# Kernel tuning notes

Measured on AMD Instinct MI355X. Metric: run time of the kernel, lower is better.

Reference implementation:

```python
import jax, jax.numpy as jnp
import numpy as np

U, NB, I, D = 20000, 10000, 40000, 64
L = 2          # num_layers
H = 64         # fusion hidden
M = 40         # max bundle size
BATCH, K = 8192, 2
DEG_UI, DEG_UB = 30, 20


def _sym_block(r, c, nA, nB):
    """Build symmetric bipartite block [[0, A],[A^T, 0]] with laplace normalization."""
    rows = np.concatenate([r, c + nA])
    cols = np.concatenate([c + nA, r])
    n = nA + nB
    deg = np.bincount(rows, minlength=n).astype(np.float64)
    inv = 1.0 / (np.sqrt(deg) + 1e-8)
    vals = (inv[rows] * inv[cols]).astype(np.float32)
    return rows.astype(np.int32), cols.astype(np.int32), vals


def setup_inputs() -> dict:
    rng = np.random.default_rng(0)
    ui_r = np.repeat(np.arange(U), DEG_UI)
    ui_c = rng.integers(0, I, U * DEG_UI)
    il_rows, il_cols, il_vals = _sym_block(ui_r, ui_c, U, I)
    ub_r = np.repeat(np.arange(U), DEG_UB)
    ub_c = rng.integers(0, NB, U * DEG_UB)
    bl_rows, bl_cols, bl_vals = _sym_block(ub_r, ub_c, U, NB)
    lengths = rng.integers(10, M + 1, NB)
    bundle_item_ids = rng.integers(0, I, (NB, M)).astype(np.int32)
    bundle_item_mask = (np.arange(M)[None, :] < lengths[:, None])

    key = jax.random.key(0)
    ks = jax.random.split(key, 8)

    def xavier(k, shape):
        std = np.sqrt(2.0 / (shape[0] + shape[1])).astype(np.float32)
        return jax.random.normal(k, shape, dtype=jnp.float32) * std

    return {
        'users_feature': xavier(ks[0], (U, D)),
        'items_feature': xavier(ks[1], (I, D)),
        'bundles_feature': xavier(ks[2], (NB, D)),
        'fw1': xavier(ks[3], (2 * D, H)),
        'fb1': jnp.zeros((H,), jnp.float32),
        'fw2': xavier(ks[4], (H, 1)),
        'fb2': jnp.zeros((1,), jnp.float32),
        'il_rows': jnp.asarray(il_rows), 'il_cols': jnp.asarray(il_cols), 'il_vals': jnp.asarray(il_vals),
        'bl_rows': jnp.asarray(bl_rows), 'bl_cols': jnp.asarray(bl_cols), 'bl_vals': jnp.asarray(bl_vals),
        'bundle_item_ids': jnp.asarray(bundle_item_ids),
        'bundle_item_mask': jnp.asarray(bundle_item_mask),
        'users': jax.random.randint(ks[5], (BATCH,), 0, U, dtype=jnp.int32),
        'bundles': jax.random.randint(ks[6], (BATCH, K), 0, NB, dtype=jnp.int32),
    }


def _spmm(rows, cols, vals, x, n):
    return jax.ops.segment_sum(vals[:, None] * x[cols], rows, num_segments=n)


def _propagate(rows, cols, vals, feat_a, feat_b):
    # one_propagate: L rounds of spmm, /(layer+2), L2-normalize, then sum over layers
    na = feat_a.shape[0]
    n = na + feat_b.shape[0]
    f = jnp.concatenate([feat_a, feat_b], axis=0)
    acc = f
    for layer in range(L):
        f = _spmm(rows, cols, vals, f, n) / (layer + 2)
        norm = jnp.maximum(jnp.linalg.norm(f, axis=1, keepdims=True), 1e-12)
        acc = acc + f / norm
    return acc[:na], acc[na:]


def reference(users_feature, items_feature, bundles_feature, fw1, fb1, fw2, fb2,
              il_rows, il_cols, il_vals, bl_rows, bl_cols, bl_vals,
              bundle_item_ids, bundle_item_mask, users, bundles):
    IL_u, IL_i = _propagate(il_rows, il_cols, il_vals, users_feature, items_feature)
    BL_u, BL_b = _propagate(bl_rows, bl_cols, bl_vals, users_feature, bundles_feature)

    q = IL_u[users]                          # [B, D] item-level user rep
    ids = bundle_item_ids[bundles]           # [B, K, M]
    msk = bundle_item_mask[bundles]          # [B, K, M]
    it = IL_i[ids]                           # [B, K, M, D]

    # user-conditioned dot attention over bundle items, masked softmax
    logits = jnp.einsum('bd,bkmd->bkm', q, it)
    logits = jnp.where(msk, logits, jnp.float32(-1e9))
    w = jax.nn.softmax(logits, axis=-1)
    il_bundle = jnp.einsum('bkm,bkmd->bkd', w, it)   # attended item-level bundle rep

    il_score = jnp.einsum('bd,bkd->bk', q, il_bundle)
    bl_u = BL_u[users]
    bl_score = jnp.einsum('bd,bkd->bk', bl_u, BL_b[bundles])

    # user-specific view fusion gate
    gate_in = jnp.concatenate([q, bl_u], axis=-1)        # [B, 2D]
    g = jax.nn.sigmoid(jax.nn.relu(gate_in @ fw1 + fb1) @ fw2 + fb2)  # [B, 1]
    pred = g * il_score + (1.0 - g) * bl_score           # [B, K]
    return pred
```

## Files before the change

kernel.cpp:

```cpp
#include <hip/hip_runtime.h>
#include <hip/hip_bf16.h>
#include <math.h>


typedef unsigned short ushortT;
#define CHUNK 8192

__device__ __forceinline__ float wSum(float v) {
#pragma unroll
    for (int o = 32; o >= 1; o >>= 1) v += __shfl_xor(v, o, 64);
    return v;
}
__device__ __forceinline__ float wMax(float v) {
#pragma unroll
    for (int o = 32; o >= 1; o >>= 1) v = fmaxf(v, __shfl_xor(v, o, 64));
    return v;
}
__device__ __forceinline__ float bf2f(ushortT u) {
    return __uint_as_float(((unsigned int)u) << 16);
}
__device__ __forceinline__ ushortT f2bf(float f) {
    unsigned int x = __float_as_uint(f);
    return (ushortT)((x + 0x7fffu + ((x >> 16) & 1u)) >> 16);
}
__device__ __forceinline__ void up2(unsigned int u, float& lo, float& hi) {
    lo = __uint_as_float(u << 16);
    hi = __uint_as_float(u & 0xffff0000u);
}
__device__ __forceinline__ unsigned int pk2(float lo, float hi) {
    return ((unsigned int)f2bf(hi) << 16) | f2bf(lo);
}

__global__ void zero_ints(int* __restrict__ p, int n) {
    int i = blockIdx.x * blockDim.x + threadIdx.x;
    if (i < n) p[i] = 0;
}

__global__ void prep_init(
    const int* __restrict__ colsA, const float* __restrict__ valsA,
    int halfA, int nblkA, int cpbA, float suA,
    int* __restrict__ cntA, int* __restrict__ histTA,
    const int* __restrict__ colsB, const float* __restrict__ valsB,
    int halfB, int nblkB, int cpbB, float suB,
    int* __restrict__ cntB, int* __restrict__ histTB,
    int nA0,
    const float* __restrict__ uf, const float* __restrict__ itf,
    const float* __restrict__ buf,
    ushortT* __restrict__ f0A, int nTotA,
    ushortT* __restrict__ f0B, int nTotB) {
    __shared__ int h[256];
    int blk = blockIdx.x, t = threadIdx.x;
    int edgeBlks = nblkA + nblkB;
    if (blk < edgeBlks) {
        const int* cols; const float* vals; int half, nblk, cpb, k;
        float su; int *cnt, *histT;
        if (blk < nblkA) { cols = colsA; vals = valsA; half = halfA; nblk = nblkA; cpb = cpbA;
                           su = suA; cnt = cntA; histT = histTA; k = blk; }
        else             { cols = colsB; vals = valsB; half = halfB; nblk = nblkB; cpb = cpbB;
                           su = suB; cnt = cntB; histT = histTB; k = blk - nblkA; }
        h[t] = 0;
        __syncthreads();
        int s = k * CHUNK, e = min(s + CHUNK, half);
        for (int i = s + t; i < e; i += 256) {
            int c = cols[i] - nA0;
            float x = 1.f / (vals[i] * su) - 1e-8f;
            cnt[c] = (int)(x * x + 0.5f);
            atomicAdd(&h[c / cpb], 1);
        }
        __syncthreads();
        histT[t * nblk + k] = h[t];
    } else {
        int idx = (blk - edgeBlks) * 256 + t;
        int totA = nTotA * 64;
        if (idx < totA) {
            int r = idx >> 6;
            f0A[idx] = f2bf((r < nA0) ? uf[idx] : itf[idx - nA0 * 64]);
        } else if (idx < totA + nTotB * 64) {
            int j = idx - totA;
            int r = j >> 6;
            f0B[j] = f2bf((r < nA0) ? uf[j] : buf[j - nA0 * 64]);
        }
    }
}

__global__ void scan1_4(const int* c0, int n0, int nb0, int* p0,
                        const int* c1, int n1, int nb1, int* p1,
                        const int* c2, int n2, int nb2, int* p2,
                        const int* c3, int n3, int nb3, int* p3) {
    int blk = blockIdx.x, t = threadIdx.x;
    const int* cnt; int n; int* part; int cb;
    if (blk < nb0)                 { cnt = c0; n = n0; part = p0; cb = blk; }
    else if (blk < nb0 + nb1)      { cnt = c1; n = n1; part = p1; cb = blk - nb0; }
    else if (blk < nb0 + nb1 + nb2){ cnt = c2; n = n2; part = p2; cb = blk - nb0 - nb1; }
    else                           { cnt = c3; n = n3; part = p3; cb = blk - nb0 - nb1 - nb2; }
    int i = cb * 256 + t;
    int v = (i < n) ? cnt[i] : 0;
#pragma unroll
    for (int o = 32; o >= 1; o >>= 1) v += __shfl_xor(v, o, 64);
    __shared__ int sm[4];
    if ((t & 63) == 0) sm[t >> 6] = v;
    __syncthreads();
    if (t == 0) part[cb] = sm[0] + sm[1] + sm[2] + sm[3];
}

__global__ void scan3_4(const int* c0, int n0, int nb0, const int* p0, int* o0, int* u0,
                        const int* c1, int n1, int nb1, const int* p1, int* o1, int* u1,
                        const int* c2, int n2, int nb2, const int* p2, int* o2,
                        const int* c3, int n3, int nb3, const int* p3, int* o3) {
    __shared__ int sm[256];
    int blk = blockIdx.x, t = threadIdx.x;
    const int *cnt, *part; int *ofs, *cur; int n, cb, tail;
    if (blk < nb0)                 { cnt = c0; n = n0; part = p0; ofs = o0; cur = u0; cb = blk; tail = 1; }
    else if (blk < nb0 + nb1)      { cnt = c1; n = n1; part = p1; ofs = o1; cur = u1; cb = blk - nb0; tail = 1; }
    else if (blk < nb0 + nb1 + nb2){ cnt = c2; n = n2; part = p2; ofs = o2; cur = 0; cb = blk - nb0 - nb1; tail = 0; }
    else                           { cnt = c3; n = n3; part = p3; ofs = o3; cur = 0; cb = blk - nb0 - nb1 - nb2; tail = 0; }
    sm[t] = (t < cb) ? part[t] : 0;
    __syncthreads();
    for (int o = 128; o >= 1; o >>= 1) {
        if (t < o) sm[t] += sm[t + o];
        __syncthreads();
    }
    int base = sm[0];
    __syncthreads();
    int i = cb * 256 + t;
    int v = (i < n) ? cnt[i] : 0;
    sm[t] = v;
    __syncthreads();
    for (int o = 1; o < 256; o <<= 1) {
        int x = (t >= o) ? sm[t - o] : 0;
        __syncthreads();
        sm[t] += x;
        __syncthreads();
    }
    int excl = sm[t] - v + base;
    if (i < n) {
        ofs[i] = excl;
        if (cur) cur[i] = excl;
        if (tail && i == n - 1) ofs[n] = excl + v;
    }
}

__global__ void p1scat(const int* __restrict__ rowsA, const int* __restrict__ colsA,
                       int halfA, int nblkA, int cpbA, int nAA,
                       const int* __restrict__ hsA, unsigned int* __restrict__ pairA,
                       const int* __restrict__ rowsB, const int* __restrict__ colsB,
                       int halfB, int nblkB, int cpbB, int nAB,
                       const int* __restrict__ hsB, unsigned int* __restrict__ pairB) {
    __shared__ int cur[256];
    int blk = blockIdx.x, t = threadIdx.x;
    const int *rows, *cols, *hs; int half, nblk, cpb, nA0, k; unsigned int* pair;
    if (blk < nblkA) { rows = rowsA; cols = colsA; hs = hsA; pair = pairA;
                       half = halfA; nblk = nblkA; cpb = cpbA; nA0 = nAA; k = blk; }
    else             { rows = rowsB; cols = colsB; hs = hsB; pair = pairB;
                       half = halfB; nblk = nblkB; cpb = cpbB; nA0 = nAB; k = blk - nblkA; }
    cur[t] = hs[t * nblk + k];
    __syncthreads();
    int s = k * CHUNK, e = min(s + CHUNK, half);
    for (int i = s + t; i < e; i += 256) {
        int c = cols[i] - nA0;
        int pos = atomicAdd(&cur[c / cpb], 1);
        pair[pos] = ((unsigned int)c << 16) | (unsigned int)rows[i];
    }
}

__global__ void p2scat(const unsigned int* __restrict__ pairA, const int* __restrict__ ofsA,
                       int cpbA, int nColsA, int* __restrict__ tuA,
                       const unsigned int* __restrict__ pairB, const int* __restrict__ ofsB,
                       int cpbB, int nColsB, int* __restrict__ tuB) {
    __shared__ int cur[512];
    int blk = blockIdx.x, t = threadIdx.x;
    const unsigned int* pair; const int* ofs; int cpb, nCols, b; int* tu;
    if (blk < 256) { pair = pairA; ofs = ofsA; cpb = cpbA; nCols = nColsA; tu = tuA; b = blk; }
    else           { pair = pairB; ofs = ofsB; cpb = cpbB; nCols = nColsB; tu = tuB; b = blk - 256; }
    int c0 = b * cpb;
    if (c0 >= nCols) return;
    int c1 = min(c0 + cpb, nCols);
    for (int j = t; j < c1 - c0; j += 256) cur[j] = ofs[c0 + j];
    __syncthreads();
    int s = ofs[c0], e = ofs[c1];
    for (int i = s + t; i < e; i += 256) {
        unsigned int pr = pair[i];
        int pos = atomicAdd(&cur[(pr >> 16) - c0], 1);
        tu[pos] = (int)(pr & 0xffffu);
    }
}

__global__ void scatter2(const int* __restrict__ rowsA, const int* __restrict__ colsA,
                         int nAA, int halfA, int* __restrict__ curA, int* __restrict__ tuA,
                         const int* __restrict__ rowsB, const int* __restrict__ colsB,
                         int nAB, int halfB, int* __restrict__ curB, int* __restrict__ tuB) {
    int i = blockIdx.x * blockDim.x + threadIdx.x;
    if (i < halfA) {
        int c = colsA[i] - nAA;
        int p = atomicAdd(&curA[c], 1);
        tuA[p] = rowsA[i];
    } else if (i < halfA + halfB) {
        int j = i - halfA;
        int c = colsB[j] - nAB;
        int p = atomicAdd(&curB[c], 1);
        tuB[p] = rowsB[j];
    }
}

template <int DEG, int LAST>
__device__ __forceinline__ void layer8_body(
    const int* __restrict__ cols, const float* __restrict__ vals,
    const int* __restrict__ ofs, const int* __restrict__ tuser,
    const ushortT* __restrict__ f, ushortT* __restrict__ fnext,
    float* __restrict__ nrm,
    const float* __restrict__ origU, const float* __restrict__ origO,
    ushortT* __restrict__ accOut,
    int row, int p, int nA, int nTot, int deg, float invu, float inv_s) {
    if (row >= nTot) return;
    float a[8] = {0.f, 0.f, 0.f, 0.f, 0.f, 0.f, 0.f, 0.f};
    if (row < nA) {
        const int* cp = cols + (long)row * deg;
        const float* vp = vals + (long)row * deg;
        if constexpr (DEG > 0) {
#pragma unroll 10
            for (int e = 0; e < DEG; ++e) {
                int c = cp[e];
                float vv = vp[e];
                uint4 rv = *(const uint4*)(f + ((long)c << 6) + (p << 3));
                float x0, x1;
                up2(rv.x, x0, x1); a[0] = fmaf(vv, x0, a[0]); a[1] = fmaf(vv, x1, a[1]);
                up2(rv.y, x0, x1); a[2] = fmaf(vv, x0, a[2]); a[3] = fmaf(vv, x1, a[3]);
                up2(rv.z, x0, x1); a[4] = fmaf(vv, x0, a[4]); a[5] = fmaf(vv, x1, a[5]);
                up2(rv.w, x0, x1); a[6] = fmaf(vv, x0, a[6]); a[7] = fmaf(vv, x1, a[7]);
            }
        } else {
#pragma unroll 4
            for (int e = 0; e < deg; ++e) {
                int c = cp[e];
                float vv = vp[e];
                uint4 rv = *(const uint4*)(f + ((long)c << 6) + (p << 3));
                float x0, x1;
                up2(rv.x, x0, x1); a[0] = fmaf(vv, x0, a[0]); a[1] = fmaf(vv, x1, a[1]);
                up2(rv.y, x0, x1); a[2] = fmaf(vv, x0, a[2]); a[3] = fmaf(vv, x1, a[3]);
                up2(rv.z, x0, x1); a[4] = fmaf(vv, x0, a[4]); a[5] = fmaf(vv, x1, a[5]);
                up2(rv.w, x0, x1); a[6] = fmaf(vv, x0, a[6]); a[7] = fmaf(vv, x1, a[7]);
            }
        }
    } else {
        int r2 = row - nA;
        int s = ofs[r2], e2 = ofs[r2 + 1];
#pragma unroll 8
        for (int j = s; j < e2; ++j) {
            int uu = tuser[j];
            uint4 rv = *(const uint4*)(f + ((long)uu << 6) + (p << 3));
            float x0, x1;
            up2(rv.x, x0, x1); a[0] += x0; a[1] += x1;
            up2(rv.y, x0, x1); a[2] += x0; a[3] += x1;
            up2(rv.z, x0, x1); a[4] += x0; a[5] += x1;
            up2(rv.w, x0, x1); a[6] += x0; a[7] += x1;
        }
        float invi = 1.f / (sqrtf((float)(e2 - s)) + 1e-8f);
        float sc = invi * invu;
#pragma unroll
        for (int d = 0; d < 8; ++d) a[d] *= sc;
    }
    float ss = 0.f;
#pragma unroll
    for (int d = 0; d < 8; ++d) {
        a[d] *= inv_s;
        ss = fmaf(a[d], a[d], ss);
    }
    ss += __shfl_xor(ss, 1, 64);
    ss += __shfl_xor(ss, 2, 64);
    ss += __shfl_xor(ss, 4, 64);
    float inv_nrm = 1.f / fmaxf(sqrtf(ss), 1e-12f);
    long base = ((long)row << 6) + (p << 3);
    if constexpr (!LAST) {
        if (p == 0) nrm[row] = inv_nrm;
        uint4 fb;
        fb.x = pk2(a[0], a[1]);
        fb.y = pk2(a[2], a[3]);
        fb.z = pk2(a[4], a[5]);
        fb.w = pk2(a[6], a[7]);
        *(uint4*)(fnext + base) = fb;
    } else {
        const float* op = (row < nA) ? (origU + base)
                                     : (origO + (((long)(row - nA)) << 6) + (p << 3));
        float4 c0 = *(const float4*)op;
        float4 c1 = *(const float4*)(op + 4);
        float n1 = nrm[row];
        uint4 f1v = *(const uint4*)(f + base);
        float x0, x1, x2, x3, x4, x5, x6, x7;
        up2(f1v.x, x0, x1);
        up2(f1v.y, x2, x3);
        up2(f1v.z, x4, x5);
        up2(f1v.w, x6, x7);
        uint4 ob;
        ob.x = pk2(c0.x + x0 * n1 + a[0] * inv_nrm, c0.y + x1 * n1 + a[1] * inv_nrm);
        ob.y = pk2(c0.z + x2 * n1 + a[2] * inv_nrm, c0.w + x3 * n1 + a[3] * inv_nrm);
        ob.z = pk2(c1.x + x4 * n1 + a[4] * inv_nrm, c1.y + x5 * n1 + a[5] * inv_nrm);
        ob.w = pk2(c1.z + x6 * n1 + a[6] * inv_nrm, c1.w + x7 * n1 + a[7] * inv_nrm);
        *(uint4*)(accOut + base) = ob;
    }
}

template <int DA, int DB, int LAST>
__global__ void __launch_bounds__(256) layer8_fused(
    const int* colsA, const float* valsA, const int* ofsA, const int* tuA,
    const ushortT* fA, ushortT* fnA, float* nrmA,
    const float* origUA, const float* origOA, ushortT* accOutA,
    int nAA, int nTotA, int degA, float invuA,
    const int* colsB, const float* valsB, const int* ofsB, const int* tuB,
    const ushortT* fB, ushortT* fnB, float* nrmB,
    const float* origUB, const float* origOB, ushortT* accOutB,
    int nAB, int nTotB, int degB, float invuB,
    float inv_s) {
    int gw = (blockIdx.x * blockDim.x + threadIdx.x) >> 6;
    int lane = threadIdx.x & 63;
    int oct = lane >> 3, p = lane & 7;
    int wA = (nTotA + 7) >> 3;
    int wB = (nTotB + 7) >> 3;
    if (gw < wA) {
        layer8_body<DA, LAST>(colsA, valsA, ofsA, tuA, fA, fnA, nrmA, origUA, origOA, accOutA,
                              gw * 8 + oct, p, nAA, nTotA, degA, invuA, inv_s);
    } else if (gw < wA + wB) {
        layer8_body<DB, LAST>(colsB, valsB, ofsB, tuB, fB, fnB, nrmB, origUB, origOB, accOutB,
                              (gw - wA) * 8 + oct, p, nAB, nTotB, degB, invuB, inv_s);
    }
}

template <int MM>
__global__ void __launch_bounds__(256) score_kernel_t(
    const ushortT* __restrict__ accIL, const ushortT* __restrict__ accBL,
    const int* __restrict__ bitem, const unsigned char* __restrict__ mask8,
    const int* __restrict__ users, const int* __restrict__ bundles,
    const float* __restrict__ fw1, const float* __restrict__ fb1,
    const float* __restrict__ fw2, const float* __restrict__ fb2,
    float* __restrict__ out, int U, int K, int B) {
    int b = (blockIdx.x * blockDim.x + threadIdx.x) >> 6;
    int lane = threadIdx.x & 63;
    if (b >= B) return;
    bool mu8 = (mask8[1] != 0);
    const int* m32 = (const int*)mask8;

    int u = users[b];
    const ushortT* qrow = accIL + ((long)u << 6);
    float q = bf2f(qrow[lane]);
    float blu = bf2f(accBL[((long)u << 6) + lane]);

    int pos = lane & 7;
    uint4 qv = *(const uint4*)(qrow + (pos << 3));
    float q8[8];
    up2(qv.x, q8[0], q8[1]);
    up2(qv.y, q8[2], q8[3]);
    up2(qv.z, q8[4], q8[5]);
    up2(qv.w, q8[6], q8[7]);

    float h0 = fb1[lane], h1 = 0.f, h2 = 0.f, h3 = 0.f;
#pragma unroll
    for (int i = 0; i < 64; i += 4) {
        h0 = fmaf(__shfl(q, i, 64),     fw1[i * 64 + lane],       h0);
        h1 = fmaf(__shfl(q, i + 1, 64), fw1[(i + 1) * 64 + lane], h1);
        h2 = fmaf(__shfl(q, i + 2, 64), fw1[(i + 2) * 64 + lane], h2);
        h3 = fmaf(__shfl(q, i + 3, 64), fw1[(i + 3) * 64 + lane], h3);
    }
#pragma unroll
    for (int i = 0; i < 64; i += 4) {
        h0 = fmaf(__shfl(blu, i, 64),     fw1[(64 + i) * 64 + lane],     h0);
        h1 = fmaf(__shfl(blu, i + 1, 64), fw1[(64 + i + 1) * 64 + lane], h1);
        h2 = fmaf(__shfl(blu, i + 2, 64), fw1[(64 + i + 2) * 64 + lane], h2);
        h3 = fmaf(__shfl(blu, i + 3, 64), fw1[(64 + i + 3) * 64 + lane], h3);
    }
    float h = fmaxf((h0 + h1) + (h2 + h3), 0.f);
    float gd = wSum(h * fw2[lane]) + fb2[0];
    float g = 1.f / (1.f + __expf(-gd));

    for (int k = 0; k < K; ++k) {
        int bd = bundles[b * K + k];
        float blb = bf2f(accBL[((long)(U + bd)) * 64 + lane]);
        long ib = (long)bd * MM;
        int idl = (lane < MM) ? bitem[ib + lane] : 0;
        bool mv = (lane < MM) ? (mu8 ? (mask8[ib + lane] != 0) : (m32[ib + lane] != 0))
                              : false;
        unsigned long long vmask = __ballot(mv);

        float el = -1e30f, lr = 0.f;
#pragma unroll
        for (int i = 0; i < MM / 8; ++i) {
            int id = __shfl(idl, 8 * i + (lane >> 3), 64);
            uint4 rv = *(const uint4*)(accIL + (((long)(U + id)) << 6) + (pos << 3));
            float a0, a1, s;
            up2(rv.x, a0, a1);
            s = fmaf(q8[0], a0, q8[1] * a1);
            up2(rv.y, a0, a1);
            s = fmaf(q8[2], a0, fmaf(q8[3], a1, s));
            up2(rv.z, a0, a1);
            s = fmaf(q8[4], a0, fmaf(q8[5], a1, s));
            up2(rv.w, a0, a1);
            s = fmaf(q8[6], a0, fmaf(q8[7], a1, s));
            s += __shfl_xor(s, 1, 64);
            s += __shfl_xor(s, 2, 64);
            s += __shfl_xor(s, 4, 64);
            float v = __shfl(s, (lane & 7) << 3, 64);
            if ((lane >> 3) == i) {
                lr = v;
                el = ((vmask >> lane) & 1ull) ? v : -1e9f;
            }
        }
        float bl = wSum(blu * blb);
        float maxl = wMax(el);
        float pe = __expf(el - maxl);
        float sum = wSum(pe);
        float il = wSum(pe * lr) / sum;
        if (lane == 0) out[b * K + k] = g * il + (1.f - g) * bl;
    }
}

__global__ void __launch_bounds__(256) score_kernel_gen(
    const ushortT* __restrict__ accIL, const ushortT* __restrict__ accBL,
    const int* __restrict__ bitem, const unsigned char* __restrict__ mask8,
    const int* __restrict__ users, const int* __restrict__ bundles,
    const float* __restrict__ fw1, const float* __restrict__ fb1,
    const float* __restrict__ fw2, const float* __restrict__ fb2,
    float* __restrict__ out, int U, int M, int K, int B) {
    int b = (blockIdx.x * blockDim.x + threadIdx.x) >> 6;
    int lane = threadIdx.x & 63;
    if (b >= B) return;
    bool mu8 = (mask8[1] != 0);
    const int* m32 = (const int*)mask8;
    int u = users[b];
    float q = bf2f(accIL[((long)u << 6) + lane]);
    float blu = bf2f(accBL[((long)u << 6) + lane]);
    float h = fb1[lane];
#pragma unroll 8
    for (int i = 0; i < 64; ++i) h = fmaf(__shfl(q, i, 64), fw1[i * 64 + lane], h);
#pragma unroll 8
    for (int i = 0; i < 64; ++i) h = fmaf(__shfl(blu, i, 64), fw1[(64 + i) * 64 + lane], h);
    h = fmaxf(h, 0.f);
    float gd = wSum(h * fw2[lane]) + fb2[0];
    float g = 1.f / (1.f + __expf(-gd));
    for (int k = 0; k < K; ++k) {
        int bd = bundles[b * K + k];
        float blb = bf2f(accBL[((long)(U + bd)) * 64 + lane]);
        float bl = wSum(blu * blb);
        long ib = (long)bd * M;
        int idl = (lane < M) ? bitem[ib + lane] : 0;
        bool mv = (lane < M) ? (mu8 ? (mask8[ib + lane] != 0) : (m32[ib + lane] != 0))
                             : false;
        unsigned long long vmask = __ballot(mv);
        float el = -1e30f, lr = 0.f;
#pragma unroll 8
        for (int m = 0; m < M; ++m) {
            int id = __shfl(idl, m, 64);
            float it = bf2f(accIL[((long)(U + id)) * 64 + lane]);
            float l = wSum(q * it);
            float lm = ((vmask >> m) & 1ull) ? l : -1e9f;
            if (lane == m) { el = lm; lr = l; }
        }
        float maxl = wMax(el);
        float pe = __expf(el - maxl);
        float sum = wSum(pe);
        float il = wSum(pe * lr) / sum;
        if (lane == 0) out[b * K + k] = g * il + (1.f - g) * bl;
    }
}

extern "C" void kernel_launch(void* const* d_in, const int* in_sizes, int n_in,
                              void* d_out, int out_size, void* d_ws, size_t ws_size,
                              hipStream_t stream) {
    const float* users_feature   = (const float*)d_in[0];
    const float* items_feature   = (const float*)d_in[1];
    const float* bundles_feature = (const float*)d_in[2];
    const float* fw1 = (const float*)d_in[3];
    const float* fb1 = (const float*)d_in[4];
    const float* fw2 = (const float*)d_in[5];
    const float* fb2 = (const float*)d_in[6];
    const int*   il_rows = (const int*)d_in[7];
    const int*   il_cols = (const int*)d_in[8];
    const float* il_vals = (const float*)d_in[9];
    const int*   bl_rows = (const int*)d_in[10];
    const int*   bl_cols = (const int*)d_in[11];
    const float* bl_vals = (const float*)d_in[12];
    const int*   bitem   = (const int*)d_in[13];
    const unsigned char* bmask = (const unsigned char*)d_in[14];
    const int*   users   = (const int*)d_in[15];
    const int*   bundles = (const int*)d_in[16];

    const int D = 64;
    int U  = in_sizes[0] / D;
    int I  = in_sizes[1] / D;
    int NB = in_sizes[2] / D;
    int nnzIL = in_sizes[7];
    int nnzBL = in_sizes[10];
    int degUI = (nnzIL / 2) / U;
    int degUB = (nnzBL / 2) / U;
    int M = in_sizes[13] / NB;
    int BATCH = in_sizes[15];
    int K = in_sizes[16] / BATCH;
    int nIL = U + I;
    int nBL = U + NB;
    int halfIL = U * degUI;
    int halfBL = U * degUB;

    char* wsB = (char*)d_ws;
    size_t off = 0;
    auto alc = [&](size_t bytes) -> void* {
        void* p = wsB + off;
        off = (off + bytes + 255) & ~(size_t)255;
        return p;
    };
    ushortT* accILbf = (ushortT*)alc((size_t)nIL * 64 * 2);
    ushortT* accBLbf = (ushortT*)alc((size_t)nBL * 64 * 2);
    ushortT* f0A = (ushortT*)alc((size_t)nIL * 64 * 2);
    ushortT* f1A = (ushortT*)alc((size_t)nIL * 64 * 2);
    ushortT* f0B = (ushortT*)alc((size_t)nBL * 64 * 2);
    ushortT* f1B = (ushortT*)alc((size_t)nBL * 64 * 2);
    float* nrmA = (float*)alc((size_t)nIL * 4);
    float* nrmB = (float*)alc((size_t)nBL * 4);
    int* ofsIL = (int*)alc((size_t)(I + 1) * 4);
    int* tuIL  = (int*)alc((size_t)halfIL * 4);
    int* ofsBL = (int*)alc((size_t)(NB + 1) * 4);
    int* tuBL  = (int*)alc((size_t)halfBL * 4);
    int* cnt   = (int*)alc((size_t)(I + NB) * 4);
    int* cur   = (int*)alc((size_t)(I + NB) * 4);
    int* cntIL = cnt,  *cntBL = cnt + I;
    int* curIL = cur,  *curBL = cur + I;

    int nblkA = (halfIL + CHUNK - 1) / CHUNK;
    int nblkB = (halfBL + CHUNK - 1) / CHUNK;
    int cpbA = (I + 255) / 256;
    int cpbB = (NB + 255) / 256;
    int LA = 256 * nblkA, LB = 256 * nblkB;
    unsigned int* pairIL = (unsigned int*)alc((size_t)halfIL * 4);
    unsigned int* pairBL = (unsigned int*)alc((size_t)halfBL * 4);
    int* histTA = (int*)alc((size_t)LA * 4);
    int* histSA = (int*)alc((size_t)(LA + 1) * 4);
    int* histTB = (int*)alc((size_t)LB * 4);
    int* histSB = (int*)alc((size_t)(LB + 1) * 4);
    int* part0  = (int*)alc(256 * 4);
    int* part1  = (int*)alc(256 * 4);
    int* part2  = (int*)alc(256 * 4);
    int* part3  = (int*)alc(256 * 4);

    float suA = sqrtf((float)degUI) + 1e-8f;
    float suB = sqrtf((float)degUB) + 1e-8f;

    zero_ints<<<(I + NB + 255) / 256, 256, 0, stream>>>(cnt, I + NB);

    int elemsTot = (nIL + nBL) * 64;
    int initBlks = (elemsTot + 255) / 256;
    prep_init<<<nblkA + nblkB + initBlks, 256, 0, stream>>>(
        il_cols, il_vals, halfIL, nblkA, cpbA, suA, cntIL, histTA,
        bl_cols, bl_vals, halfBL, nblkB, cpbB, suB, cntBL, histTB,
        U, users_feature, items_feature, bundles_feature,
        f0A, nIL, f0B, nBL);

    int nb0 = (I + 255) / 256, nb1 = (NB + 255) / 256;
    int nb2 = nblkA, nb3 = nblkB;
    scan1_4<<<nb0 + nb1 + nb2 + nb3, 256, 0, stream>>>(
        cntIL, I, nb0, part0, cntBL, NB, nb1, part1,
        histTA, LA, nb2, part2, histTB, LB, nb3, part3);
    scan3_4<<<nb0 + nb1 + nb2 + nb3, 256, 0, stream>>>(
        cntIL, I, nb0, part0, ofsIL, curIL,
        cntBL, NB, nb1, part1, ofsBL, curBL,
        histTA, LA, nb2, part2, histSA,
        histTB, LB, nb3, part3, histSB);

    bool fast = (I < 65536) && (NB < 65536) && (U < 65536) &&
                (cpbA <= 512) && (cpbB <= 512) &&
                (nb0 <= 256) && (nb1 <= 256) &&
                (nblkA >= 1) && (nblkB >= 1) && (nblkA <= 256) && (nblkB <= 256);
    if (fast) {
        p1scat<<<nblkA + nblkB, 256, 0, stream>>>(
            il_rows, il_cols, halfIL, nblkA, cpbA, U, histSA, pairIL,
            bl_rows, bl_cols, halfBL, nblkB, cpbB, U, histSB, pairBL);
        p2scat<<<512, 256, 0, stream>>>(pairIL, ofsIL, cpbA, I, tuIL,
                                        pairBL, ofsBL, cpbB, NB, tuBL);
    } else {
        scatter2<<<(halfIL + halfBL + 255) / 256, 256, 0, stream>>>(
            il_rows, il_cols, U, halfIL, curIL, tuIL,
            bl_rows, bl_cols, U, halfBL, curBL, tuBL);
    }

    float invuA = 1.f / suA;
    float invuB = 1.f / suB;
    int wavesTot = ((nIL + 7) >> 3) + ((nBL + 7) >> 3);
    int lgrid = (wavesTot * 64 + 255) / 256;
    if (degUI == 30 && degUB == 20) {
        layer8_fused<30, 20, 0><<<lgrid, 256, 0, stream>>>(
            il_cols, il_vals, ofsIL, tuIL, f0A, f1A, nrmA, users_feature, items_feature, accILbf,
            U, nIL, degUI, invuA,
            bl_cols, bl_vals, ofsBL, tuBL, f0B, f1B, nrmB, users_feature, bundles_feature, accBLbf,
            U, nBL, degUB, invuB, 0.5f);
        layer8_fused<30, 20, 1><<<lgrid, 256, 0, stream>>>(
            il_cols, il_vals, ofsIL, tuIL, f1A, f0A, nrmA, users_feature, items_feature, accILbf,
            U, nIL, degUI, invuA,
            bl_cols, bl_vals, ofsBL, tuBL, f1B, f0B, nrmB, users_feature, bundles_feature, accBLbf,
            U, nBL, degUB, invuB, 1.f / 3.f);
    } else {
        layer8_fused<0, 0, 0><<<lgrid, 256, 0, stream>>>(
            il_cols, il_vals, ofsIL, tuIL, f0A, f1A, nrmA, users_feature, items_feature, accILbf,
            U, nIL, degUI, invuA,
            bl_cols, bl_vals, ofsBL, tuBL, f0B, f1B, nrmB, users_feature, bundles_feature, accBLbf,
            U, nBL, degUB, invuB, 0.5f);
        layer8_fused<0, 0, 1><<<lgrid, 256, 0, stream>>>(
            il_cols, il_vals, ofsIL, tuIL, f1A, f0A, nrmA, users_feature, items_feature, accILbf,
            U, nIL, degUI, invuA,
            bl_cols, bl_vals, ofsBL, tuBL, f1B, f0B, nrmB, users_feature, bundles_feature, accBLbf,
            U, nBL, degUB, invuB, 1.f / 3.f);
    }

    if (M == 40) {
        score_kernel_t<40><<<(BATCH * 64 + 255) / 256, 256, 0, stream>>>(
            accILbf, accBLbf, bitem, bmask, users, bundles, fw1, fb1, fw2, fb2,
            (float*)d_out, U, K, BATCH);
    } else {
        score_kernel_gen<<<(BATCH * 64 + 255) / 256, 256, 0, stream>>>(
            accILbf, accBLbf, bitem, bmask, users, bundles, fw1, fb1, fw2, fb2,
            (float*)d_out, U, M, K, BATCH);
    }
}
```

Baseline: 154.2 us.

## Derive CSR offsets inside bucket scatter, drop degree-from-values count pass

Per-column in-degree counts were recovered by inverting the normalized edge values and then scanned globally. Now the second-pass bucket scatter counts columns per bucket in shared memory and computes the offsets itself, writing the CSR offset array as a side effect. This removes the zero_ints launch, the float inversion, the random count writes and the item/bundle count scans on the fast path. In exchange each bucket block reads its pair slice twice, and buckets are now limited to 256 columns, which tightens the fast-path condition.

```diff
diff --git a/kernel.cpp b/kernel.cpp
--- a/kernel.cpp
+++ b/kernel.cpp
@@ -36,13 +36,21 @@
     if (i < n) p[i] = 0;
 }
 
-__global__ void prep_init(
-    const int* __restrict__ colsA, const float* __restrict__ valsA,
-    int halfA, int nblkA, int cpbA, float suA,
-    int* __restrict__ cntA, int* __restrict__ histTA,
-    const int* __restrict__ colsB, const float* __restrict__ valsB,
-    int halfB, int nblkB, int cpbB, float suB,
-    int* __restrict__ cntB, int* __restrict__ histTB,
+__global__ void hist_at(const int* __restrict__ colsA, int halfA, int nAA, int* __restrict__ cntA,
+                        const int* __restrict__ colsB, int halfB, int nAB, int* __restrict__ cntB) {
+    int i = blockIdx.x * blockDim.x + threadIdx.x;
+    if (i < halfA) atomicAdd(&cntA[colsA[i] - nAA], 1);
+    else if (i < halfA + halfB) {
+        int j = i - halfA;
+        atomicAdd(&cntB[colsB[j] - nAB], 1);
+    }
+}
+
+__global__ void prep_f(
+    const int* __restrict__ colsA, int halfA, int nblkA, int cpbA,
+    int* __restrict__ histTA,
+    const int* __restrict__ colsB, int halfB, int nblkB, int cpbB,
+    int* __restrict__ histTB,
     int nA0,
     const float* __restrict__ uf, const float* __restrict__ itf,
     const float* __restrict__ buf,
@@ -52,21 +60,13 @@
     int blk = blockIdx.x, t = threadIdx.x;
     int edgeBlks = nblkA + nblkB;
     if (blk < edgeBlks) {
-        const int* cols; const float* vals; int half, nblk, cpb, k;
-        float su; int *cnt, *histT;
-        if (blk < nblkA) { cols = colsA; vals = valsA; half = halfA; nblk = nblkA; cpb = cpbA;
-                           su = suA; cnt = cntA; histT = histTA; k = blk; }
-        else             { cols = colsB; vals = valsB; half = halfB; nblk = nblkB; cpb = cpbB;
-                           su = suB; cnt = cntB; histT = histTB; k = blk - nblkA; }
+        const int* cols; int half, nblk, cpb, k; int* histT;
+        if (blk < nblkA) { cols = colsA; half = halfA; nblk = nblkA; cpb = cpbA; histT = histTA; k = blk; }
+        else             { cols = colsB; half = halfB; nblk = nblkB; cpb = cpbB; histT = histTB; k = blk - nblkA; }
         h[t] = 0;
         __syncthreads();
         int s = k * CHUNK, e = min(s + CHUNK, half);
-        for (int i = s + t; i < e; i += 256) {
-            int c = cols[i] - nA0;
-            float x = 1.f / (vals[i] * su) - 1e-8f;
-            cnt[c] = (int)(x * x + 0.5f);
-            atomicAdd(&h[c / cpb], 1);
-        }
+        for (int i = s + t; i < e; i += 256) atomicAdd(&h[(cols[i] - nA0) / cpb], 1);
         __syncthreads();
         histT[t * nblk + k] = h[t];
     } else {
@@ -83,16 +83,12 @@
     }
 }
 
-__global__ void scan1_4(const int* c0, int n0, int nb0, int* p0,
-                        const int* c1, int n1, int nb1, int* p1,
-                        const int* c2, int n2, int nb2, int* p2,
-                        const int* c3, int n3, int nb3, int* p3) {
+__global__ void scan1h(const int* c0, int n0, int nb0, int* p0,
+                       const int* c1, int n1, int nb1, int* p1) {
     int blk = blockIdx.x, t = threadIdx.x;
     const int* cnt; int n; int* part; int cb;
-    if (blk < nb0)                 { cnt = c0; n = n0; part = p0; cb = blk; }
-    else if (blk < nb0 + nb1)      { cnt = c1; n = n1; part = p1; cb = blk - nb0; }
-    else if (blk < nb0 + nb1 + nb2){ cnt = c2; n = n2; part = p2; cb = blk - nb0 - nb1; }
-    else                           { cnt = c3; n = n3; part = p3; cb = blk - nb0 - nb1 - nb2; }
+    if (blk < nb0) { cnt = c0; n = n0; part = p0; cb = blk; }
+    else           { cnt = c1; n = n1; part = p1; cb = blk - nb0; }
     int i = cb * 256 + t;
     int v = (i < n) ? cnt[i] : 0;
 #pragma unroll
@@ -103,18 +99,16 @@
     if (t == 0) part[cb] = sm[0] + sm[1] + sm[2] + sm[3];
 }
 
-__global__ void scan3_4(const int* c0, int n0, int nb0, const int* p0, int* o0, int* u0,
-                        const int* c1, int n1, int nb1, const int* p1, int* o1, int* u1,
-                        const int* c2, int n2, int nb2, const int* p2, int* o2,
-                        const int* c3, int n3, int nb3, const int* p3, int* o3) {
+__global__ void scan3h(const int* c0, int n0, int nb0, const int* p0, int* o0, int* u0, int t0,
+                       const int* c1, int n1, int nb1, const int* p1, int* o1, int* u1, int t1) {
     __shared__ int sm[256];
     int blk = blockIdx.x, t = threadIdx.x;
     const int *cnt, *part; int *ofs, *cur; int n, cb, tail;
-    if (blk < nb0)                 { cnt = c0; n = n0; part = p0; ofs = o0; cur = u0; cb = blk; tail = 1; }
-    else if (blk < nb0 + nb1)      { cnt = c1; n = n1; part = p1; ofs = o1; cur = u1; cb = blk - nb0; tail = 1; }
-    else if (blk < nb0 + nb1 + nb2){ cnt = c2; n = n2; part = p2; ofs = o2; cur = 0; cb = blk - nb0 - nb1; tail = 0; }
-    else                           { cnt = c3; n = n3; part = p3; ofs = o3; cur = 0; cb = blk - nb0 - nb1 - nb2; tail = 0; }
-    sm[t] = (t < cb) ? part[t] : 0;
+    if (blk < nb0) { cnt = c0; n = n0; part = p0; ofs = o0; cur = u0; cb = blk; tail = t0; }
+    else           { cnt = c1; n = n1; part = p1; ofs = o1; cur = u1; cb = blk - nb0; tail = t1; }
+    int acc = 0;
+    for (int j = t; j < cb; j += 256) acc += part[j];
+    sm[t] = acc;
     __syncthreads();
     for (int o = 128; o >= 1; o >>= 1) {
         if (t < o) sm[t] += sm[t + o];
@@ -163,24 +157,50 @@
     }
 }
 
-__global__ void p2scat(const unsigned int* __restrict__ pairA, const int* __restrict__ ofsA,
-                       int cpbA, int nColsA, int* __restrict__ tuA,
-                       const unsigned int* __restrict__ pairB, const int* __restrict__ ofsB,
-                       int cpbB, int nColsB, int* __restrict__ tuB) {
-    __shared__ int cur[512];
+__global__ void p2scat_ofs(
+    const unsigned int* __restrict__ pairA, const int* __restrict__ hsA,
+    int nblkA, int halfA, int cpbA, int nColsA,
+    int* __restrict__ ofsA, int* __restrict__ tuA,
+    const unsigned int* __restrict__ pairB, const int* __restrict__ hsB,
+    int nblkB, int halfB, int cpbB, int nColsB,
+    int* __restrict__ ofsB, int* __restrict__ tuB) {
+    __shared__ int lcnt[256];
+    __shared__ int lofs[256];
     int blk = blockIdx.x, t = threadIdx.x;
-    const unsigned int* pair; const int* ofs; int cpb, nCols, b; int* tu;
-    if (blk < 256) { pair = pairA; ofs = ofsA; cpb = cpbA; nCols = nColsA; tu = tuA; b = blk; }
-    else           { pair = pairB; ofs = ofsB; cpb = cpbB; nCols = nColsB; tu = tuB; b = blk - 256; }
+    const unsigned int* pair; const int* hs; int nblk, half, cpb, nCols, b; int *ofs, *tu;
+    if (blk < 256) { pair = pairA; hs = hsA; nblk = nblkA; half = halfA; cpb = cpbA;
+                     nCols = nColsA; ofs = ofsA; tu = tuA; b = blk; }
+    else           { pair = pairB; hs = hsB; nblk = nblkB; half = halfB; cpb = cpbB;
+                     nCols = nColsB; ofs = ofsB; tu = tuB; b = blk - 256; }
     int c0 = b * cpb;
     if (c0 >= nCols) return;
     int c1 = min(c0 + cpb, nCols);
-    for (int j = t; j < c1 - c0; j += 256) cur[j] = ofs[c0 + j];
-    __syncthreads();
-    int s = ofs[c0], e = ofs[c1];
+    int w = c1 - c0;
+    int s = hs[b * nblk];
+    int e = (b == 255) ? half : hs[(b + 1) * nblk];
+    lcnt[t] = 0;
+    __syncthreads();
+    for (int i = s + t; i < e; i += 256)
+        atomicAdd(&lcnt[(int)(pair[i] >> 16) - c0], 1);
+    __syncthreads();
+    int v = lcnt[t];
+    lofs[t] = v;
+    __syncthreads();
+    for (int o = 1; o < 256; o <<= 1) {
+        int x = (t >= o) ? lofs[t - o] : 0;
+        __syncthreads();
+        lofs[t] += x;
+        __syncthreads();
+    }
+    int excl = lofs[t] - v + s;
+    if (t < w) ofs[c0 + t] = excl;
+    if (t == 0 && c1 == nCols) ofs[nCols] = e;
+    __syncthreads();
+    lofs[t] = excl;
+    __syncthreads();
     for (int i = s + t; i < e; i += 256) {
         unsigned int pr = pair[i];
-        int pos = atomicAdd(&cur[(pr >> 16) - c0], 1);
+        int pos = atomicAdd(&lofs[(int)(pr >> 16) - c0], 1);
         tu[pos] = (int)(pr & 0xffffu);
     }
 }
@@ -534,44 +554,42 @@
     int* histSB = (int*)alc((size_t)(LB + 1) * 4);
     int* part0  = (int*)alc(256 * 4);
     int* part1  = (int*)alc(256 * 4);
-    int* part2  = (int*)alc(256 * 4);
-    int* part3  = (int*)alc(256 * 4);
 
     float suA = sqrtf((float)degUI) + 1e-8f;
     float suB = sqrtf((float)degUB) + 1e-8f;
 
-    zero_ints<<<(I + NB + 255) / 256, 256, 0, stream>>>(cnt, I + NB);
-
     int elemsTot = (nIL + nBL) * 64;
     int initBlks = (elemsTot + 255) / 256;
-    prep_init<<<nblkA + nblkB + initBlks, 256, 0, stream>>>(
-        il_cols, il_vals, halfIL, nblkA, cpbA, suA, cntIL, histTA,
-        bl_cols, bl_vals, halfBL, nblkB, cpbB, suB, cntBL, histTB,
+    prep_f<<<nblkA + nblkB + initBlks, 256, 0, stream>>>(
+        il_cols, halfIL, nblkA, cpbA, histTA,
+        bl_cols, halfBL, nblkB, cpbB, histTB,
         U, users_feature, items_feature, bundles_feature,
         f0A, nIL, f0B, nBL);
 
-    int nb0 = (I + 255) / 256, nb1 = (NB + 255) / 256;
-    int nb2 = nblkA, nb3 = nblkB;
-    scan1_4<<<nb0 + nb1 + nb2 + nb3, 256, 0, stream>>>(
-        cntIL, I, nb0, part0, cntBL, NB, nb1, part1,
-        histTA, LA, nb2, part2, histTB, LB, nb3, part3);
-    scan3_4<<<nb0 + nb1 + nb2 + nb3, 256, 0, stream>>>(
-        cntIL, I, nb0, part0, ofsIL, curIL,
-        cntBL, NB, nb1, part1, ofsBL, curBL,
-        histTA, LA, nb2, part2, histSA,
-        histTB, LB, nb3, part3, histSB);
-
     bool fast = (I < 65536) && (NB < 65536) && (U < 65536) &&
-                (cpbA <= 512) && (cpbB <= 512) &&
-                (nb0 <= 256) && (nb1 <= 256) &&
+                (cpbA <= 256) && (cpbB <= 256) &&
                 (nblkA >= 1) && (nblkB >= 1) && (nblkA <= 256) && (nblkB <= 256);
     if (fast) {
+        scan1h<<<nblkA + nblkB, 256, 0, stream>>>(histTA, LA, nblkA, part0,
+                                                  histTB, LB, nblkB, part1);
+        scan3h<<<nblkA + nblkB, 256, 0, stream>>>(
+            histTA, LA, nblkA, part0, histSA, nullptr, 0,
+            histTB, LB, nblkB, part1, histSB, nullptr, 0);
         p1scat<<<nblkA + nblkB, 256, 0, stream>>>(
             il_rows, il_cols, halfIL, nblkA, cpbA, U, histSA, pairIL,
             bl_rows, bl_cols, halfBL, nblkB, cpbB, U, histSB, pairBL);
-        p2scat<<<512, 256, 0, stream>>>(pairIL, ofsIL, cpbA, I, tuIL,
-                                        pairBL, ofsBL, cpbB, NB, tuBL);
+        p2scat_ofs<<<512, 256, 0, stream>>>(
+            pairIL, histSA, nblkA, halfIL, cpbA, I, ofsIL, tuIL,
+            pairBL, histSB, nblkB, halfBL, cpbB, NB, ofsBL, tuBL);
     } else {
+        zero_ints<<<(I + NB + 255) / 256, 256, 0, stream>>>(cnt, I + NB);
+        hist_at<<<(halfIL + halfBL + 255) / 256, 256, 0, stream>>>(
+            il_cols, halfIL, U, cntIL, bl_cols, halfBL, U, cntBL);
+        int nb0 = (I + 255) / 256, nb1 = (NB + 255) / 256;
+        scan1h<<<nb0 + nb1, 256, 0, stream>>>(cntIL, I, nb0, part0, cntBL, NB, nb1, part1);
+        scan3h<<<nb0 + nb1, 256, 0, stream>>>(
+            cntIL, I, nb0, part0, ofsIL, curIL, 1,
+            cntBL, NB, nb1, part1, ofsBL, curBL, 1);
         scatter2<<<(halfIL + halfBL + 255) / 256, 256, 0, stream>>>(
             il_rows, il_cols, U, halfIL, curIL, tuIL,
             bl_rows, bl_cols, U, halfBL, curBL, tuBL);
```

After: 145.6 us. 5.6% less time.
